# Performance work log

Measured on AMD Instinct MI355X. Metric: run time of the kernel, lower is better.

The kernel has to match this reference:

```python
import jax, jax.numpy as jnp
import numpy as np

DIM = 768
NUM_HEADS = 12
HEAD_DIM = DIM // NUM_HEADS
SCALE = HEAD_DIM ** -0.5
N, B = 1024, 8


def setup_inputs() -> dict:
    key = jax.random.key(0)
    ks = jax.random.split(key, 10)
    s = 0.02
    return {
        "q": jax.random.normal(ks[0], (N, B, DIM), jnp.float32),
        "k": jax.random.normal(ks[1], (N, B, DIM), jnp.float32),
        "v": jax.random.normal(ks[2], (N, B, DIM), jnp.float32),
        "v_img": jax.random.normal(ks[3], (N, B, DIM), jnp.float32),
        "Wq": jax.random.normal(ks[4], (DIM, DIM), jnp.float32) * s,
        "Wk": jax.random.normal(ks[5], (DIM, DIM), jnp.float32) * s,
        "Wv": jax.random.normal(ks[6], (DIM, DIM), jnp.float32) * s,
        "Wvim": jax.random.normal(ks[7], (DIM, DIM), jnp.float32) * s,
        "Wp": jax.random.normal(ks[8], (DIM, DIM), jnp.float32) * s,
        "bp": jnp.zeros((DIM,), jnp.float32),
        "Wpi": jax.random.normal(ks[9], (DIM, DIM), jnp.float32) * s,
        "bpi": jnp.zeros((DIM,), jnp.float32),
    }


def _heads(x):
    # [B, N, C] -> [B, H, N, Dh]
    b, n, _ = x.shape
    return x.reshape(b, n, NUM_HEADS, HEAD_DIM).transpose(0, 2, 1, 3)


def _merge(x):
    # [B, H, N, Dh] -> [B, N, C]
    b, h, n, d = x.shape
    return x.transpose(0, 2, 1, 3).reshape(b, n, h * d)


def reference(q, k, v, v_img, Wq, Wk, Wv, Wvim, Wp, bp, Wpi, bpi):
    # seq-first [N, B, C] -> batch-first [B, N, C]
    qb = jnp.transpose(q, (1, 0, 2)) @ Wq.T
    kb = jnp.transpose(k, (1, 0, 2)) @ Wk.T
    vb = jnp.transpose(v, (1, 0, 2)) @ Wv.T
    vib = jnp.transpose(v_img, (1, 0, 2)) @ Wvim.T

    qh, kh, vh, vih = _heads(qb), _heads(kb), _heads(vb), _heads(vib)

    # shared attention matrix, reused for both value streams
    attn = jnp.einsum("bhqd,bhkd->bhqk", qh, kh) * SCALE
    attn = jax.nn.softmax(attn, axis=-1)

    x = _merge(jnp.einsum("bhqk,bhkd->bhqd", attn, vh)) @ Wp.T + bp
    x_im = _merge(jnp.einsum("bhqk,bhkd->bhqd", attn, vih)) @ Wpi.T + bpi
    return (x, x_im)
```

## Files before the change

### kernel.cpp

```cpp
#include <hip/hip_runtime.h>

#define NSEQ 1024
#define BATCH 8
#define DIMC 768
#define NH 12
#define HD 64
#define SEG 6291456
#define WSEG 589824

typedef __attribute__((ext_vector_type(4))) float f32x4;
typedef __attribute__((ext_vector_type(8))) short s16x8;
typedef __attribute__((ext_vector_type(8))) __bf16 bf16x8;

#define GLL16(gsrc, ldst) __builtin_amdgcn_global_load_lds( \
    (const __attribute__((address_space(1))) unsigned int*)(const void*)(gsrc), \
    (__attribute__((address_space(3))) unsigned int*)(void*)(ldst), 16, 0, 0)

__device__ __forceinline__ short f2bf(float f) {
  union { float f; unsigned u; } v; v.f = f;
  unsigned r = (v.u + 0x7FFFu + ((v.u >> 16) & 1u)) >> 16;
  return (short)r;
}

__device__ __forceinline__ f32x4 mfma16(bf16x8 a, bf16x8 b, f32x4 c) {
  return __builtin_amdgcn_mfma_f32_16x16x32_bf16(a, b, c, 0, 0, 0);
}

__global__ __launch_bounds__(256) void k_cvt4(
    const float* __restrict__ a0, const float* __restrict__ a1,
    const float* __restrict__ a2, const float* __restrict__ a3,
    short* __restrict__ b0, short* __restrict__ b1,
    short* __restrict__ b2, short* __restrict__ b3, int n4) {
  const float* src; short* dst;
  switch (blockIdx.y) {
    case 0: src = a0; dst = b0; break;
    case 1: src = a1; dst = b1; break;
    case 2: src = a2; dst = b2; break;
    default: src = a3; dst = b3; break;
  }
  int i = blockIdx.x * 256 + threadIdx.x;
  if (i >= n4) return;
  float4 f = reinterpret_cast<const float4*>(src)[i];
  short4 o;
  o.x = f2bf(f.x); o.y = f2bf(f.y); o.z = f2bf(f.z); o.w = f2bf(f.w);
  reinterpret_cast<short4*>(dst)[i] = o;
}

__global__ __launch_bounds__(256) void k_proj(
    const short* __restrict__ x0, const short* __restrict__ x1,
    const short* __restrict__ x2, const short* __restrict__ x3,
    const short* __restrict__ w0, const short* __restrict__ w1,
    const short* __restrict__ w2, const short* __restrict__ w3,
    short* __restrict__ y0, short* __restrict__ y1,
    short* __restrict__ y2, short* __restrict__ y3) {
  __shared__ __align__(16) short SM[32768];
  const int tid = threadIdx.x;
  const int lane = tid & 63;
  const int w = tid >> 6;
  const int wm = w >> 1, wn = w & 1;
  const int mt = blockIdx.x, nt = blockIdx.y, s = blockIdx.z;
  const short *X, *W; short* Y;
  if (s == 0)      { X = x0; W = w0; Y = y0; }
  else if (s == 1) { X = x1; W = w1; Y = y1; }
  else if (s == 2) { X = x2; W = w2; Y = y2; }
  else             { X = x3; W = w3; Y = y3; }

  f32x4 acc[4][4];
#pragma unroll
  for (int mi = 0; mi < 4; ++mi)
#pragma unroll
    for (int ni = 0; ni < 4; ++ni) acc[mi][ni] = (f32x4){0.f, 0.f, 0.f, 0.f};

#define PROJ_STAGE(BUF, KT) do { \
  _Pragma("unroll") for (int ii = 0; ii < 4; ++ii) { \
    int g = ii * 256 + tid; \
    int o = g * 16; \
    int r = o >> 7; \
    int c0 = ((o & 127) ^ ((r & 7) << 4)) >> 1; \
    int m = mt * 128 + r; \
    GLL16(X + ((size_t)((m & 1023) * BATCH + (m >> 10))) * DIMC + (KT) * 64 + c0, \
          (char*)(SM + (BUF) * 8192) + o); \
    GLL16(W + (size_t)(nt * 128 + r) * DIMC + (KT) * 64 + c0, \
          (char*)(SM + 16384 + (BUF) * 8192) + o); \
  } \
} while (0)

  PROJ_STAGE(0, 0);
  __syncthreads();
  int buf = 0;
  for (int kt = 0; kt < 12; ++kt) {
    if (kt < 11) PROJ_STAGE(buf ^ 1, kt + 1);
    const char* As = (const char*)(SM + buf * 8192);
    const char* Bs = (const char*)(SM + 16384 + buf * 8192);
#pragma unroll
    for (int kk = 0; kk < 2; ++kk) {
      bf16x8 a[4], b[4];
      int ce = kk * 32 + (lane >> 4) * 8;
#pragma unroll
      for (int mi = 0; mi < 4; ++mi) {
        int ra = wm * 64 + mi * 16 + (lane & 15);
        int byte = ((ra << 7) + (ce << 1)) ^ ((ra & 7) << 4);
        a[mi] = *(const bf16x8*)(As + byte);
      }
#pragma unroll
      for (int ni = 0; ni < 4; ++ni) {
        int rb = wn * 64 + ni * 16 + (lane & 15);
        int byte = ((rb << 7) + (ce << 1)) ^ ((rb & 7) << 4);
        b[ni] = *(const bf16x8*)(Bs + byte);
      }
#pragma unroll
      for (int mi = 0; mi < 4; ++mi)
#pragma unroll
        for (int ni = 0; ni < 4; ++ni)
          acc[mi][ni] = mfma16(a[mi], b[ni], acc[mi][ni]);
    }
    __syncthreads();
    buf ^= 1;
  }
#undef PROJ_STAGE

  if (s < 2) {
#pragma unroll
    for (int mi = 0; mi < 4; ++mi)
#pragma unroll
      for (int ni = 0; ni < 4; ++ni)
#pragma unroll
        for (int j = 0; j < 4; ++j) {
          int m = mt * 128 + wm * 64 + mi * 16 + (lane >> 4) * 4 + j;
          int dc = nt * 128 + wn * 64 + ni * 16 + (lane & 15);
          int b_ = m >> 10, n_ = m & 1023;
          int h_ = dc >> 6, d_ = dc & 63;
          Y[((size_t)(b_ * NH + h_) * NSEQ + n_) * HD + d_] = f2bf(acc[mi][ni][j]);
        }
  } else {
    short* Ts = SM;
#pragma unroll
    for (int mi = 0; mi < 4; ++mi)
#pragma unroll
      for (int ni = 0; ni < 4; ++ni)
#pragma unroll
        for (int j = 0; j < 4; ++j) {
          int lm = wm * 64 + mi * 16 + (lane >> 4) * 4 + j;
          int ldc = wn * 64 + ni * 16 + (lane & 15);
          int swc = ldc ^ (lm & 126);
          Ts[lm * 128 + swc] = f2bf(acc[mi][ni][j]);
        }
    __syncthreads();
    int l2 = lane * 2;
#pragma unroll 4
    for (int it = 0; it < 32; ++it) {
      int ldc = it * 4 + w;
      short2 pk;
      pk.x = Ts[l2 * 128 + (ldc ^ (l2 & 126))];
      pk.y = Ts[(l2 + 1) * 128 + (ldc ^ ((l2 + 1) & 126))];
      int dc = nt * 128 + ldc;
      int h_ = dc >> 6, d_ = dc & 63;
      int m = mt * 128 + l2;
      int b_ = m >> 10, n_ = m & 1023;
      *(short2*)(Y + ((size_t)(b_ * NH + h_) * HD + d_) * NSEQ + n_) = pk;
    }
  }
}

__global__ __launch_bounds__(256) void k_attn(
    const short* __restrict__ qh, const short* __restrict__ kh,
    const short* __restrict__ vt, const short* __restrict__ vit,
    short* __restrict__ xo, short* __restrict__ xio) {
  __shared__ __align__(16) short Ks[2][4096];
  __shared__ __align__(16) short Vs[2][4096];
  __shared__ __align__(16) short Vis[2][4096];
  __shared__ __align__(16) short Pl[4][2048];

  const int tid = threadIdx.x;
  const int lane = tid & 63;
  const int w = tid >> 6;
  const int blk = blockIdx.x;
  const int virt = (blk & 7) * 96 + (blk >> 3);
  const int bh = virt >> 3;
  const int qt = virt & 7;
  const float CF = 0.125f * 1.44269504f;

  const short* qbase = qh + ((size_t)bh * NSEQ + qt * 128 + w * 32) * HD;
  bf16x8 qf[2][2];
#pragma unroll
  for (int mi = 0; mi < 2; ++mi)
#pragma unroll
    for (int kq = 0; kq < 2; ++kq)
      qf[mi][kq] = *(const bf16x8*)(qbase + (mi * 16 + (lane & 15)) * HD + kq * 32 + (lane >> 4) * 8);

  bf16x8 onesf;
#pragma unroll
  for (int i = 0; i < 8; ++i) onesf[i] = (__bf16)1.0f;

  f32x4 o_[2][4], oi_[2][4], l_acc[2];
#pragma unroll
  for (int mi = 0; mi < 2; ++mi) {
    l_acc[mi] = (f32x4){0.f, 0.f, 0.f, 0.f};
#pragma unroll
    for (int x = 0; x < 4; ++x) {
      o_[mi][x] = (f32x4){0.f, 0.f, 0.f, 0.f};
      oi_[mi][x] = (f32x4){0.f, 0.f, 0.f, 0.f};
    }
  }

  const short* khb = kh + (size_t)bh * NSEQ * HD;
  const short* vtb = vt + (size_t)bh * NSEQ * HD;
  const short* vitb = vit + (size_t)bh * NSEQ * HD;
  char* PlW = (char*)&Pl[w][0];

#define ATTN_STAGE(BUF, KT) do { \
  _Pragma("unroll") for (int ii = 0; ii < 2; ++ii) { \
    int g = ii * 256 + tid; \
    int o = g * 16; \
    int r = o >> 7; \
    int c0 = ((o & 127) ^ ((r & 7) << 4)) >> 1; \
    GLL16(khb + (size_t)((KT) * 64 + r) * HD + c0, (char*)&Ks[BUF][0] + o); \
    GLL16(vtb + (size_t)r * NSEQ + (KT) * 64 + c0, (char*)&Vs[BUF][0] + o); \
    GLL16(vitb + (size_t)r * NSEQ + (KT) * 64 + c0, (char*)&Vis[BUF][0] + o); \
  } \
} while (0)

  ATTN_STAGE(0, 0);
  __syncthreads();
  int buf = 0;
  for (int kt = 0; kt < 16; ++kt) {
    if (kt < 15) ATTN_STAGE(buf ^ 1, kt + 1);
    const char* KsB = (const char*)&Ks[buf][0];
    const char* VsB = (const char*)&Vs[buf][0];
    const char* VisB = (const char*)&Vis[buf][0];

#pragma unroll
    for (int ni = 0; ni < 4; ++ni) {
      f32x4 s0 = (f32x4){0.f, 0.f, 0.f, 0.f};
      f32x4 s1 = (f32x4){0.f, 0.f, 0.f, 0.f};
#pragma unroll
      for (int kk = 0; kk < 2; ++kk) {
        int ce = kk * 32 + (lane >> 4) * 8;
        int rb = ni * 16 + (lane & 15);
        int byte = ((rb << 7) + (ce << 1)) ^ ((rb & 7) << 4);
        bf16x8 kfr = *(const bf16x8*)(KsB + byte);
        s0 = mfma16(qf[0][kk], kfr, s0);
        s1 = mfma16(qf[1][kk], kfr, s1);
      }
#pragma unroll
      for (int j = 0; j < 4; ++j) {
        float p0 = exp2f(s0[j] * CF);
        float p1 = exp2f(s1[j] * CF);
        int rw0 = (lane >> 4) * 4 + j;
        int col = ni * 16 + (lane & 15);
        int b0 = ((rw0 << 7) + (col << 1)) ^ ((rw0 & 7) << 4);
        int b1 = (((rw0 + 16) << 7) + (col << 1)) ^ ((rw0 & 7) << 4);
        *(short*)(PlW + b0) = f2bf(p0);
        *(short*)(PlW + b1) = f2bf(p1);
      }
    }

#pragma unroll
    for (int kk = 0; kk < 2; ++kk) {
      int co = kk * 32 + (lane >> 4) * 8;
      int r0 = lane & 15;
      int bp0 = ((r0 << 7) + (co << 1)) ^ ((r0 & 7) << 4);
      int bp1 = (((r0 + 16) << 7) + (co << 1)) ^ ((r0 & 7) << 4);
      bf16x8 pa0 = *(const bf16x8*)(PlW + bp0);
      bf16x8 pa1 = *(const bf16x8*)(PlW + bp1);
      l_acc[0] = mfma16(pa0, onesf, l_acc[0]);
      l_acc[1] = mfma16(pa1, onesf, l_acc[1]);
#pragma unroll
      for (int nd = 0; nd < 4; ++nd) {
        int rv = nd * 16 + (lane & 15);
        int byte = ((rv << 7) + (co << 1)) ^ ((rv & 7) << 4);
        bf16x8 vb = *(const bf16x8*)(VsB + byte);
        bf16x8 vib = *(const bf16x8*)(VisB + byte);
        o_[0][nd] = mfma16(pa0, vb, o_[0][nd]);
        o_[1][nd] = mfma16(pa1, vb, o_[1][nd]);
        oi_[0][nd] = mfma16(pa0, vib, oi_[0][nd]);
        oi_[1][nd] = mfma16(pa1, vib, oi_[1][nd]);
      }
    }
    __syncthreads();
    buf ^= 1;
  }
#undef ATTN_STAGE

#pragma unroll
  for (int mi = 0; mi < 2; ++mi)
#pragma unroll
    for (int j = 0; j < 4; ++j) {
      float inv = 1.0f / l_acc[mi][j];
      int n_ = qt * 128 + w * 32 + mi * 16 + (lane >> 4) * 4 + j;
      size_t base = ((size_t)bh * NSEQ + n_) * HD;
#pragma unroll
      for (int nd = 0; nd < 4; ++nd) {
        int d_ = nd * 16 + (lane & 15);
        xo[base + d_] = f2bf(o_[mi][nd][j] * inv);
        xio[base + d_] = f2bf(oi_[mi][nd][j] * inv);
      }
    }
}

__global__ __launch_bounds__(256) void k_outproj(
    const short* __restrict__ xa, const short* __restrict__ xb,
    const short* __restrict__ wa, const short* __restrict__ wb,
    const float* __restrict__ ba, const float* __restrict__ bb,
    float* __restrict__ out) {
  __shared__ __align__(16) short SM[32768];
  const int tid = threadIdx.x;
  const int lane = tid & 63;
  const int w = tid >> 6;
  const int wm = w >> 1, wn = w & 1;
  const int mt = blockIdx.x, nt = blockIdx.y, s = blockIdx.z;
  const short* X = (s == 0) ? xa : xb;
  const short* W = (s == 0) ? wa : wb;
  const float* bias = (s == 0) ? ba : bb;
  float* O = out + (size_t)s * SEG;

  f32x4 acc[4][4];
#pragma unroll
  for (int mi = 0; mi < 4; ++mi)
#pragma unroll
    for (int ni = 0; ni < 4; ++ni) acc[mi][ni] = (f32x4){0.f, 0.f, 0.f, 0.f};

#define OUTP_STAGE(BUF, KT) do { \
  _Pragma("unroll") for (int ii = 0; ii < 4; ++ii) { \
    int g = ii * 256 + tid; \
    int o = g * 16; \
    int r = o >> 7; \
    int c0 = ((o & 127) ^ ((r & 7) << 4)) >> 1; \
    int m = mt * 128 + r; \
    GLL16(X + (((size_t)(m >> 10) * NH + (KT)) * NSEQ + (m & 1023)) * HD + c0, \
          (char*)(SM + (BUF) * 8192) + o); \
    GLL16(W + (size_t)(nt * 128 + r) * DIMC + (KT) * 64 + c0, \
          (char*)(SM + 16384 + (BUF) * 8192) + o); \
  } \
} while (0)

  OUTP_STAGE(0, 0);
  __syncthreads();
  int buf = 0;
  for (int kt = 0; kt < 12; ++kt) {
    if (kt < 11) OUTP_STAGE(buf ^ 1, kt + 1);
    const char* As = (const char*)(SM + buf * 8192);
    const char* Bs = (const char*)(SM + 16384 + buf * 8192);
#pragma unroll
    for (int kk = 0; kk < 2; ++kk) {
      bf16x8 a[4], b[4];
      int ce = kk * 32 + (lane >> 4) * 8;
#pragma unroll
      for (int mi = 0; mi < 4; ++mi) {
        int ra = wm * 64 + mi * 16 + (lane & 15);
        int byte = ((ra << 7) + (ce << 1)) ^ ((ra & 7) << 4);
        a[mi] = *(const bf16x8*)(As + byte);
      }
#pragma unroll
      for (int ni = 0; ni < 4; ++ni) {
        int rb = wn * 64 + ni * 16 + (lane & 15);
        int byte = ((rb << 7) + (ce << 1)) ^ ((rb & 7) << 4);
        b[ni] = *(const bf16x8*)(Bs + byte);
      }
#pragma unroll
      for (int mi = 0; mi < 4; ++mi)
#pragma unroll
        for (int ni = 0; ni < 4; ++ni)
          acc[mi][ni] = mfma16(a[mi], b[ni], acc[mi][ni]);
    }
    __syncthreads();
    buf ^= 1;
  }
#undef OUTP_STAGE

#pragma unroll
  for (int mi = 0; mi < 4; ++mi)
#pragma unroll
    for (int ni = 0; ni < 4; ++ni)
#pragma unroll
      for (int j = 0; j < 4; ++j) {
        int m = mt * 128 + wm * 64 + mi * 16 + (lane >> 4) * 4 + j;
        int dc = nt * 128 + wn * 64 + ni * 16 + (lane & 15);
        O[(size_t)m * DIMC + dc] = acc[mi][ni][j] + bias[dc];
      }
}

extern "C" void kernel_launch(void* const* d_in, const int* in_sizes, int n_in,
                              void* d_out, int out_size, void* d_ws, size_t ws_size,
                              hipStream_t stream) {
  (void)in_sizes; (void)n_in; (void)out_size; (void)ws_size;
  const float* q    = (const float*)d_in[0];
  const float* k    = (const float*)d_in[1];
  const float* v    = (const float*)d_in[2];
  const float* vimg = (const float*)d_in[3];
  const float* Wq   = (const float*)d_in[4];
  const float* Wk   = (const float*)d_in[5];
  const float* Wv   = (const float*)d_in[6];
  const float* Wvim = (const float*)d_in[7];
  const float* Wp   = (const float*)d_in[8];
  const float* bp   = (const float*)d_in[9];
  const float* Wpi  = (const float*)d_in[10];
  const float* bpi  = (const float*)d_in[11];

  short* ws = (short*)d_ws;
  short* xq  = ws;
  short* xk  = ws + (size_t)SEG;
  short* xv  = ws + (size_t)2 * SEG;
  short* xvi = ws + (size_t)3 * SEG;
  short* wqb  = ws + (size_t)4 * SEG;
  short* wkb  = wqb + WSEG;
  short* wvb  = wkb + WSEG;
  short* wvib = wvb + WSEG;
  short* wpb  = wvib + WSEG;
  short* wpib = wpb + WSEG;
  short* qh  = ws + (size_t)4 * SEG + 6 * (size_t)WSEG;
  short* kh  = qh + (size_t)SEG;
  short* vht = kh + (size_t)SEG;
  short* viht = vht + (size_t)SEG;
  short* xo  = viht + (size_t)SEG;
  short* xio = xo + (size_t)SEG;

  k_cvt4<<<dim3(SEG / 4 / 256, 4), 256, 0, stream>>>(q, k, v, vimg, xq, xk, xv, xvi, SEG / 4);
  k_cvt4<<<dim3(WSEG / 4 / 256, 4), 256, 0, stream>>>(Wq, Wk, Wv, Wvim, wqb, wkb, wvb, wvib, WSEG / 4);
  k_cvt4<<<dim3(WSEG / 4 / 256, 2), 256, 0, stream>>>(Wp, Wpi, Wp, Wpi, wpb, wpib, wpb, wpib, WSEG / 4);

  k_proj<<<dim3(64, 6, 4), 256, 0, stream>>>(xq, xk, xv, xvi, wqb, wkb, wvb, wvib, qh, kh, vht, viht);

  k_attn<<<dim3(768), 256, 0, stream>>>(qh, kh, vht, viht, xo, xio);

  k_outproj<<<dim3(64, 6, 2), 256, 0, stream>>>(xo, xio, wpb, wpib, bp, bpi, (float*)d_out);
}
```

Baseline: 315.9 us.

## Load V fragments directly from global into registers and use hardware bf16 convert

The attention kernel stops staging V and V_img tiles through double-buffered LDS. Each wave now loads its MFMA B-operand fragments straight from global memory at the start of each key tile. It also swaps the software round-to-nearest bf16 conversion for the v_cvt_pk_bf16_f32 instruction. This frees LDS and cuts LDS traffic, which may allow higher occupancy. The cost is that every wave redundantly fetches the same V data from global/L2, and those loads are not prefetched ahead of use the way the LDS pipeline was, so latency may be exposed.

```diff
diff --git a/kernel.cpp b/kernel.cpp
--- a/kernel.cpp
+++ b/kernel.cpp
@@ -19,6 +19,12 @@
 __device__ __forceinline__ short f2bf(float f) {
   union { float f; unsigned u; } v; v.f = f;
   unsigned r = (v.u + 0x7FFFu + ((v.u >> 16) & 1u)) >> 16;
+  return (short)r;
+}
+
+__device__ __forceinline__ short f2bf1(float f) {
+  unsigned r;
+  asm("v_cvt_pk_bf16_f32 %0, %1, %2" : "=v"(r) : "v"(f), "v"(0.f));
   return (short)r;
 }
 
@@ -167,8 +173,6 @@
     const short* __restrict__ vt, const short* __restrict__ vit,
     short* __restrict__ xo, short* __restrict__ xio) {
   __shared__ __align__(16) short Ks[2][4096];
-  __shared__ __align__(16) short Vs[2][4096];
-  __shared__ __align__(16) short Vis[2][4096];
   __shared__ __align__(16) short Pl[4][2048];
 
   const int tid = threadIdx.x;
@@ -215,8 +219,6 @@
     int r = o >> 7; \
     int c0 = ((o & 127) ^ ((r & 7) << 4)) >> 1; \
     GLL16(khb + (size_t)((KT) * 64 + r) * HD + c0, (char*)&Ks[BUF][0] + o); \
-    GLL16(vtb + (size_t)r * NSEQ + (KT) * 64 + c0, (char*)&Vs[BUF][0] + o); \
-    GLL16(vitb + (size_t)r * NSEQ + (KT) * 64 + c0, (char*)&Vis[BUF][0] + o); \
   } \
 } while (0)
 
@@ -226,8 +228,18 @@
   for (int kt = 0; kt < 16; ++kt) {
     if (kt < 15) ATTN_STAGE(buf ^ 1, kt + 1);
     const char* KsB = (const char*)&Ks[buf][0];
-    const char* VsB = (const char*)&Vs[buf][0];
-    const char* VisB = (const char*)&Vis[buf][0];
+
+    bf16x8 vfr[2][4], vifr[2][4];
+#pragma unroll
+    for (int kk = 0; kk < 2; ++kk) {
+      int co = kk * 32 + (lane >> 4) * 8;
+#pragma unroll
+      for (int nd = 0; nd < 4; ++nd) {
+        size_t off = (size_t)(nd * 16 + (lane & 15)) * NSEQ + kt * 64 + co;
+        vfr[kk][nd]  = *(const bf16x8*)(vtb + off);
+        vifr[kk][nd] = *(const bf16x8*)(vitb + off);
+      }
+    }
 
 #pragma unroll
     for (int ni = 0; ni < 4; ++ni) {
@@ -250,8 +262,8 @@
         int col = ni * 16 + (lane & 15);
         int b0 = ((rw0 << 7) + (col << 1)) ^ ((rw0 & 7) << 4);
         int b1 = (((rw0 + 16) << 7) + (col << 1)) ^ ((rw0 & 7) << 4);
-        *(short*)(PlW + b0) = f2bf(p0);
-        *(short*)(PlW + b1) = f2bf(p1);
+        *(short*)(PlW + b0) = f2bf1(p0);
+        *(short*)(PlW + b1) = f2bf1(p1);
       }
     }
 
@@ -267,14 +279,10 @@
       l_acc[1] = mfma16(pa1, onesf, l_acc[1]);
 #pragma unroll
       for (int nd = 0; nd < 4; ++nd) {
-        int rv = nd * 16 + (lane & 15);
-        int byte = ((rv << 7) + (co << 1)) ^ ((rv & 7) << 4);
-        bf16x8 vb = *(const bf16x8*)(VsB + byte);
-        bf16x8 vib = *(const bf16x8*)(VisB + byte);
-        o_[0][nd] = mfma16(pa0, vb, o_[0][nd]);
-        o_[1][nd] = mfma16(pa1, vb, o_[1][nd]);
-        oi_[0][nd] = mfma16(pa0, vib, oi_[0][nd]);
-        oi_[1][nd] = mfma16(pa1, vib, oi_[1][nd]);
+        o_[0][nd] = mfma16(pa0, vfr[kk][nd], o_[0][nd]);
+        o_[1][nd] = mfma16(pa1, vfr[kk][nd], o_[1][nd]);
+        oi_[0][nd] = mfma16(pa0, vifr[kk][nd], oi_[0][nd]);
+        oi_[1][nd] = mfma16(pa1, vifr[kk][nd], oi_[1][nd]);
       }
     }
     __syncthreads();
@@ -292,8 +300,8 @@
 #pragma unroll
       for (int nd = 0; nd < 4; ++nd) {
         int d_ = nd * 16 + (lane & 15);
-        xo[base + d_] = f2bf(o_[mi][nd][j] * inv);
-        xio[base + d_] = f2bf(oi_[mi][nd][j] * inv);
+        xo[base + d_] = f2bf1(o_[mi][nd][j] * inv);
+        xio[base + d_] = f2bf1(oi_[mi][nd][j] * inv);
       }
     }
 }
```

After: 370.5 us. 17.3% more time.
